# Kernel optimization log

Measured on AMD Instinct MI355X. Metric: run time of the kernel, lower is better.

## Reference

```python
import jax, jax.numpy as jnp
import numpy as np

B, S, D, H = 2, 2048, 1024, 16
HD = D // H  # head_dim = 64


def setup_inputs() -> dict:
    key = jax.random.key(0)
    ks = jax.random.split(key, 9)
    s = 1.0 / np.sqrt(D)
    return {
        "x": jax.random.normal(ks[0], (B, S, D), dtype=jnp.float32),
        "Wq": jax.random.uniform(ks[1], (D, D), jnp.float32, -s, s),
        "bq": jnp.zeros((D,), jnp.float32),
        "Wk": jax.random.uniform(ks[2], (D, D), jnp.float32, -s, s),
        "bk": jnp.zeros((D,), jnp.float32),
        "Wv": jax.random.uniform(ks[3], (D, D), jnp.float32, -s, s),
        "bv": jnp.zeros((D,), jnp.float32),
        "Wo": jax.random.uniform(ks[4], (D, D), jnp.float32, -s, s),
        "bo": jnp.zeros((D,), jnp.float32),
    }


def reference(x, Wq, bq, Wk, bk, Wv, bv, Wo, bo):
    # x: [B,S,D] -> Q/K/V: [B,H,S,HD]
    def heads(t):
        return t.reshape(B, S, H, HD).transpose(0, 2, 1, 3)

    Q = heads(x @ Wq + bq)
    K = heads(x @ Wk + bk)
    V = heads(x @ Wv + bv)
    scale = jnp.sqrt(jnp.asarray(HD, dtype=x.dtype))
    energy = jnp.einsum("bhqd,bhkd->bhqk", Q, K) / scale  # [B,H,S,S]
    attn = jax.nn.softmax(energy, axis=-1)
    # dropout is identity in eval mode
    o = jnp.einsum("bhqk,bhkd->bhqd", attn, V)  # [B,H,S,HD]
    o = o.transpose(0, 2, 1, 3).reshape(B, S, D)
    return o @ Wo + bo
```

## Files before the change

### kernel.cpp

```cpp
#include <hip/hip_runtime.h>
#include <hip/hip_bf16.h>

#define B_  2
#define S_  2048
#define D_  1024
#define H_  16
#define HD_ 64

typedef __attribute__((ext_vector_type(8))) short bf16x8;
typedef __attribute__((ext_vector_type(4))) short bf16x4;
typedef __attribute__((ext_vector_type(4))) float f32x4;

typedef __attribute__((address_space(1))) const short gbl_short;
typedef __attribute__((address_space(3))) short lds_short;

__device__ __forceinline__ short f2bf(float f) {
  union { float f; unsigned u; } v; v.f = f;
  unsigned r = (v.u + 0x7FFFu + ((v.u >> 16) & 1u)) >> 16;
  return (short)r;
}

__device__ __forceinline__ short bf16s(float f) {
  __hip_bfloat16 h = __float2bfloat16(f);
  return *reinterpret_cast<short*>(&h);
}

__global__ __launch_bounds__(256) void cast_x_kernel(const float* __restrict__ x,
                                                     short* __restrict__ xb) {
  int i = blockIdx.x * 256 + threadIdx.x;
  float4 v = ((const float4*)x)[i];
  short4 o;
  o.x = f2bf(v.x); o.y = f2bf(v.y); o.z = f2bf(v.z); o.w = f2bf(v.w);
  ((short4*)xb)[i] = o;
}

__global__ __launch_bounds__(256) void transpose_cast_w(
    const float* __restrict__ w0, const float* __restrict__ w1,
    const float* __restrict__ w2, const float* __restrict__ w3,
    short* __restrict__ t0, short* __restrict__ t1,
    short* __restrict__ t2, short* __restrict__ t3) {
  const float* W = blockIdx.z == 0 ? w0 : blockIdx.z == 1 ? w1 : blockIdx.z == 2 ? w2 : w3;
  short* T       = blockIdx.z == 0 ? t0 : blockIdx.z == 1 ? t1 : blockIdx.z == 2 ? t2 : t3;
  __shared__ float tile[32][33];
  int tx = threadIdx.x, ty = threadIdx.y;
  int x0 = blockIdx.x * 32, y0 = blockIdx.y * 32;
#pragma unroll
  for (int i = 0; i < 4; ++i)
    tile[ty + i * 8][tx] = W[(y0 + ty + i * 8) * D_ + x0 + tx];
  __syncthreads();
#pragma unroll
  for (int i = 0; i < 4; ++i)
    T[(x0 + ty + i * 8) * D_ + y0 + tx] = f2bf(tile[tx][ty + i * 8]);
}

__global__ __launch_bounds__(256) void qkv_gemm(
    const short* __restrict__ xb,
    const short* __restrict__ Wqt, const short* __restrict__ Wkt, const short* __restrict__ Wvt,
    const float* __restrict__ bq, const float* __restrict__ bk, const float* __restrict__ bv,
    short* __restrict__ Qb, short* __restrict__ Kb, short* __restrict__ Vtb) {
  const int which = blockIdx.z;
  const short* Bt   = which == 0 ? Wqt : which == 1 ? Wkt : Wvt;
  const float* bias = which == 0 ? bq  : which == 1 ? bk  : bv;
  const float scl   = which == 0 ? 0.125f * 1.44269504089f : 1.0f;
  const int lane = threadIdx.x & 63, wave = threadIdx.x >> 6;
  const int l15 = lane & 15, quad = lane >> 4;
  const int wm = wave & 1, wn = wave >> 1;
  const int m0 = blockIdx.x * 128, n0 = blockIdx.y * 128;
  const int srow = lane >> 2;
  const int skp  = (((lane & 3) ^ ((srow >> 1) & 3)) * 8);
  const int rsw  = (l15 >> 1) & 3;

  __shared__ short lA[3][128 * 32];
  __shared__ short lB[3][128 * 32];

  f32x4 acc[4][4];
#pragma unroll
  for (int mi = 0; mi < 4; ++mi)
#pragma unroll
    for (int ni = 0; ni < 4; ++ni) { f32x4 z = {0.f, 0.f, 0.f, 0.f}; acc[mi][ni] = z; }

  auto stage = [&](int it, int buf) {
    int kk = it * 32;
#pragma unroll
    for (int j = 0; j < 2; ++j) {
      int c = wave * 2 + j;
      int row = c * 16 + srow;
      __builtin_amdgcn_global_load_lds(
          (gbl_short*)(xb + (m0 + row) * D_ + kk + skp),
          (lds_short*)(&lA[buf][0] + c * 512 + lane * 8), 16, 0, 0);
      __builtin_amdgcn_global_load_lds(
          (gbl_short*)(Bt + (n0 + row) * D_ + kk + skp),
          (lds_short*)(&lB[buf][0] + c * 512 + lane * 8), 16, 0, 0);
    }
  };

  auto compute = [&](int cur) {
    bf16x8 af[4], bf[4];
#pragma unroll
    for (int i = 0; i < 4; ++i) {
      af[i] = *(const bf16x8*)(&lA[cur][0] + (wm * 64 + i * 16 + l15) * 32 + ((quad ^ rsw)) * 8);
      bf[i] = *(const bf16x8*)(&lB[cur][0] + (wn * 64 + i * 16 + l15) * 32 + ((quad ^ rsw)) * 8);
    }
#pragma unroll
    for (int mi = 0; mi < 4; ++mi)
#pragma unroll
      for (int ni = 0; ni < 4; ++ni)
        acc[mi][ni] = __builtin_amdgcn_mfma_f32_16x16x32_bf16(af[mi], bf[ni], acc[mi][ni], 0, 0, 0);
  };

  stage(0, 0);
  stage(1, 1);
  for (int it = 0; it < 30; ++it) {
    stage(it + 2, (it + 2) % 3);
    asm volatile("s_waitcnt vmcnt(8)" ::: "memory");
    __builtin_amdgcn_s_barrier();
    compute(it % 3);
    asm volatile("" ::: "memory");
    __builtin_amdgcn_s_barrier();
  }
  asm volatile("s_waitcnt vmcnt(4)" ::: "memory");
  __builtin_amdgcn_s_barrier();
  compute(0);
  asm volatile("s_waitcnt vmcnt(0)" ::: "memory");
  __builtin_amdgcn_s_barrier();
  compute(1);

#pragma unroll
  for (int mi = 0; mi < 4; ++mi) {
    int m = m0 + wm * 64 + mi * 16 + quad * 4;
    int bb = m >> 11;
    int s0 = m & (S_ - 1);
#pragma unroll
    for (int ni = 0; ni < 4; ++ni) {
      int n = n0 + wn * 64 + ni * 16 + l15;
      int h = n >> 6, hd = n & 63;
      float bsv = bias[n];
      if (which < 2) {
        short* dst = which == 0 ? Qb : Kb;
#pragma unroll
        for (int r = 0; r < 4; ++r)
          dst[((bb * H_ + h) * S_ + (s0 + r)) * HD_ + hd] = f2bf((acc[mi][ni][r] + bsv) * scl);
      } else {
        short4 pk;
        pk.x = f2bf(acc[mi][ni][0] + bsv);
        pk.y = f2bf(acc[mi][ni][1] + bsv);
        pk.z = f2bf(acc[mi][ni][2] + bsv);
        pk.w = f2bf(acc[mi][ni][3] + bsv);
        *(short4*)(Vtb + ((bb * H_ + h) * HD_ + hd) * S_ + s0) = pk;
      }
    }
  }
}

__global__ __launch_bounds__(256) void out_gemm(
    const short* __restrict__ Ob, const short* __restrict__ Wot,
    const float* __restrict__ bo, float* __restrict__ out) {
  const int lane = threadIdx.x & 63, wave = threadIdx.x >> 6;
  const int l15 = lane & 15, quad = lane >> 4;
  const int wm = wave & 1, wn = wave >> 1;
  const int m0 = blockIdx.x * 128, n0 = blockIdx.y * 128;
  const int srow = lane >> 2;
  const int skp  = (((lane & 3) ^ ((srow >> 1) & 3)) * 8);
  const int rsw  = (l15 >> 1) & 3;

  __shared__ short lA[3][128 * 32];
  __shared__ short lB[3][128 * 32];

  f32x4 acc[4][4];
#pragma unroll
  for (int mi = 0; mi < 4; ++mi)
#pragma unroll
    for (int ni = 0; ni < 4; ++ni) { f32x4 z = {0.f, 0.f, 0.f, 0.f}; acc[mi][ni] = z; }

  auto stage = [&](int it, int buf) {
    int kk = it * 32;
#pragma unroll
    for (int j = 0; j < 2; ++j) {
      int c = wave * 2 + j;
      int row = c * 16 + srow;
      __builtin_amdgcn_global_load_lds(
          (gbl_short*)(Ob + (m0 + row) * D_ + kk + skp),
          (lds_short*)(&lA[buf][0] + c * 512 + lane * 8), 16, 0, 0);
      __builtin_amdgcn_global_load_lds(
          (gbl_short*)(Wot + (n0 + row) * D_ + kk + skp),
          (lds_short*)(&lB[buf][0] + c * 512 + lane * 8), 16, 0, 0);
    }
  };

  auto compute = [&](int cur) {
    bf16x8 af[4], bf[4];
#pragma unroll
    for (int i = 0; i < 4; ++i) {
      af[i] = *(const bf16x8*)(&lA[cur][0] + (wm * 64 + i * 16 + l15) * 32 + ((quad ^ rsw)) * 8);
      bf[i] = *(const bf16x8*)(&lB[cur][0] + (wn * 64 + i * 16 + l15) * 32 + ((quad ^ rsw)) * 8);
    }
#pragma unroll
    for (int mi = 0; mi < 4; ++mi)
#pragma unroll
      for (int ni = 0; ni < 4; ++ni)
        acc[mi][ni] = __builtin_amdgcn_mfma_f32_16x16x32_bf16(af[mi], bf[ni], acc[mi][ni], 0, 0, 0);
  };

  stage(0, 0);
  stage(1, 1);
  for (int it = 0; it < 30; ++it) {
    stage(it + 2, (it + 2) % 3);
    asm volatile("s_waitcnt vmcnt(8)" ::: "memory");
    __builtin_amdgcn_s_barrier();
    compute(it % 3);
    asm volatile("" ::: "memory");
    __builtin_amdgcn_s_barrier();
  }
  asm volatile("s_waitcnt vmcnt(4)" ::: "memory");
  __builtin_amdgcn_s_barrier();
  compute(0);
  asm volatile("s_waitcnt vmcnt(0)" ::: "memory");
  __builtin_amdgcn_s_barrier();
  compute(1);

#pragma unroll
  for (int mi = 0; mi < 4; ++mi) {
    int m = m0 + wm * 64 + mi * 16 + quad * 4;
#pragma unroll
    for (int ni = 0; ni < 4; ++ni) {
      int n = n0 + wn * 64 + ni * 16 + l15;
      float bsv = bo[n];
#pragma unroll
      for (int r = 0; r < 4; ++r)
        out[(m + r) * D_ + n] = acc[mi][ni][r] + bsv;
    }
  }
}

__global__ __launch_bounds__(256, 2) void attn_kernel(
    const short* __restrict__ Qb, const short* __restrict__ Kb,
    const short* __restrict__ Vtb, short* __restrict__ Ob) {
  const int qt = blockIdx.x, h = blockIdx.y, b = blockIdx.z;
  const int base = (b * H_ + h) * S_ * HD_;
  const int tid = threadIdx.x;
  const int lane = tid & 63, wave = tid >> 6;
  const int grp = wave >> 1;
  const int wq  = wave & 1;
  const int l15 = lane & 15, quad = lane >> 4;

  __shared__ __align__(16) char smem[33280];
  short* lK = (short*)smem;
  short* lV = (short*)(smem + 16384);

  const int q0 = qt * 128 + wq * 64;

  bf16x8 qf[4][2];
#pragma unroll
  for (int mi = 0; mi < 4; ++mi)
#pragma unroll
    for (int ks = 0; ks < 2; ++ks)
      qf[mi][ks] = *(const bf16x8*)(Qb + base + (q0 + mi * 16 + l15) * HD_ + ks * 32 + quad * 8);

  f32x4 oacc[4][4];
  f32x4 lacc[4];
#pragma unroll
  for (int mi = 0; mi < 4; ++mi) {
    f32x4 z = {0.f, 0.f, 0.f, 0.f};
    lacc[mi] = z;
#pragma unroll
    for (int nb = 0; nb < 4; ++nb) oacc[mi][nb] = z;
  }

  bf16x8 onesf;
#pragma unroll
  for (int i = 0; i < 8; ++i) onesf[i] = (short)0x3F80;

  const int tig = tid & 127;
  const int slotK = tig & 7,  rowK = tig >> 3;
  const int slotV = tig & 3,  rowV = tig >> 2;
  const short* kp = Kb + base + (grp * 1024 + rowK) * HD_ + ((slotK ^ (rowK & 7)) * 8);
  const short* vp = Vtb + base + rowV * S_ + grp * 1024 + ((slotV ^ ((rowV >> 2) & 3)) * 8);
  lds_short* ldk = (lds_short*)(lK + grp * 2048 + tig * 8);
  lds_short* ldv = (lds_short*)(lV + grp * 2048 + tig * 8);

  auto stage = [&](int kt, int buf) {
#pragma unroll
    for (int j = 0; j < 2; ++j) {
      __builtin_amdgcn_global_load_lds((gbl_short*)(kp + kt * 32 * HD_ + j * 16 * HD_),
                                       ldk + buf * 4096 + j * 1024, 16, 0, 0);
      __builtin_amdgcn_global_load_lds((gbl_short*)(vp + kt * 32 + j * 32 * S_),
                                       ldv + buf * 4096 + j * 1024, 16, 0, 0);
    }
  };

  const int swzK = l15 & 7;
  const int fsw  = (l15 >> 2) & 3;
  const int g1 = (quad >> 1) ^ fsw;
  const int g2 = (2 | (quad >> 1)) ^ fsw;
  const int vsub = (quad & 1) * 4;

  stage(0, 0);
  __syncthreads();

  for (int kt = 0; kt < 32; ++kt) {
    const int buf = kt & 1;
    if (kt < 31) stage(kt + 1, buf ^ 1);

    const short* lKc = lK + buf * 4096 + grp * 2048;
    const short* lVc = lV + buf * 4096 + grp * 2048;

    f32x4 sacc[4][2];
#pragma unroll
    for (int mi = 0; mi < 4; ++mi)
#pragma unroll
      for (int nb = 0; nb < 2; ++nb) { f32x4 z = {0.f, 0.f, 0.f, 0.f}; sacc[mi][nb] = z; }
#pragma unroll
    for (int nb = 0; nb < 2; ++nb)
#pragma unroll
      for (int ks = 0; ks < 2; ++ks) {
        bf16x8 kf = *(const bf16x8*)(lKc + (nb * 16 + l15) * 64 + (((ks * 4 + quad) ^ swzK) * 8));
#pragma unroll
        for (int mi = 0; mi < 4; ++mi)
          sacc[mi][nb] = __builtin_amdgcn_mfma_f32_16x16x32_bf16(kf, qf[mi][ks], sacc[mi][nb], 0, 0, 0);
      }

    bf16x8 af[4];
#pragma unroll
    for (int mi = 0; mi < 4; ++mi)
#pragma unroll
      for (int j = 0; j < 8; ++j)
        af[mi][j] = bf16s(__builtin_amdgcn_exp2f(sacc[mi][j >> 2][j & 3]));

#pragma unroll
    for (int nbh = 0; nbh < 4; ++nbh) {
      const short* vrow = lVc + (nbh * 16 + l15) * 32 + vsub;
      bf16x4 v1 = *(const bf16x4*)(vrow + g1 * 8);
      bf16x4 v2 = *(const bf16x4*)(vrow + g2 * 8);
      bf16x8 vf = __builtin_shufflevector(v1, v2, 0, 1, 2, 3, 4, 5, 6, 7);
#pragma unroll
      for (int mi = 0; mi < 4; ++mi)
        oacc[mi][nbh] = __builtin_amdgcn_mfma_f32_16x16x32_bf16(af[mi], vf, oacc[mi][nbh], 0, 0, 0);
    }
#pragma unroll
    for (int mi = 0; mi < 4; ++mi)
      lacc[mi] = __builtin_amdgcn_mfma_f32_16x16x32_bf16(af[mi], onesf, lacc[mi], 0, 0, 0);
    __syncthreads();
  }

  float* exch = (float*)smem;
  float* lex  = (float*)(smem + 32768);
  if (grp == 1) {
#pragma unroll
    for (int mi = 0; mi < 4; ++mi)
#pragma unroll
      for (int nbh = 0; nbh < 4; ++nbh)
#pragma unroll
        for (int r = 0; r < 4; ++r)
          exch[wq * 4096 + (mi * 16 + quad * 4 + r) * 64 + nbh * 16 + l15] = oacc[mi][nbh][r];
    if (l15 == 0) {
#pragma unroll
      for (int mi = 0; mi < 4; ++mi)
#pragma unroll
        for (int r = 0; r < 4; ++r)
          lex[wq * 64 + mi * 16 + quad * 4 + r] = lacc[mi][r];
    }
  }
  __syncthreads();
  if (grp == 0) {
#pragma unroll
    for (int mi = 0; mi < 4; ++mi)
#pragma unroll
      for (int r = 0; r < 4; ++r) {
        int row = mi * 16 + quad * 4 + r;
        float l2 = lex[wq * 64 + row];
        float inv = 1.0f / (lacc[mi][r] + l2);
        int sg = q0 + row;
#pragma unroll
        for (int nbh = 0; nbh < 4; ++nbh) {
          float o2 = exch[wq * 4096 + row * 64 + nbh * 16 + l15];
          Ob[(b * S_ + sg) * D_ + h * HD_ + nbh * 16 + l15] =
              bf16s((oacc[mi][nbh][r] + o2) * inv);
        }
      }
  }
}

extern "C" void kernel_launch(void* const* d_in, const int* in_sizes, int n_in,
                              void* d_out, int out_size, void* d_ws, size_t ws_size,
                              hipStream_t stream) {
  (void)in_sizes; (void)n_in; (void)out_size; (void)ws_size;
  const float* x  = (const float*)d_in[0];
  const float* Wq = (const float*)d_in[1];
  const float* bq = (const float*)d_in[2];
  const float* Wk = (const float*)d_in[3];
  const float* bk = (const float*)d_in[4];
  const float* Wv = (const float*)d_in[5];
  const float* bv = (const float*)d_in[6];
  const float* Wo = (const float*)d_in[7];
  const float* bo = (const float*)d_in[8];
  float* out = (float*)d_out;

  char* ws = (char*)d_ws;
  short* xb  = (short*)(ws);
  short* Wqt = (short*)(ws + 8388608);
  short* Wkt = Wqt + 1048576;
  short* Wvt = Wkt + 1048576;
  short* Wot = Wvt + 1048576;
  short* Qb  = Wot + 1048576;
  short* Kb  = Qb + 4194304;
  short* Vtb = Kb + 4194304;
  short* Ob  = Vtb + 4194304;

  cast_x_kernel<<<4096, 256, 0, stream>>>(x, xb);
  transpose_cast_w<<<dim3(32, 32, 4), dim3(32, 8), 0, stream>>>(
      Wq, Wk, Wv, Wo, Wqt, Wkt, Wvt, Wot);
  qkv_gemm<<<dim3(32, 8, 3), 256, 0, stream>>>(
      xb, Wqt, Wkt, Wvt, bq, bk, bv, Qb, Kb, Vtb);
  attn_kernel<<<dim3(16, 16, 2), 256, 0, stream>>>(Qb, Kb, Vtb, Ob);
  out_gemm<<<dim3(32, 8), 256, 0, stream>>>(Ob, Wot, bo, out);
}
```

Measured before the change: 188.2 us.

## Triple-buffer attention K/V staging with vmcnt waits, XCD-aware block mapping, setprio

The attention kernel's K/V staging moves from a double buffer with a full __syncthreads per tile to a three-deep ring buffer. Explicit s_waitcnt vmcnt counts and raw barriers let loads run two tiles ahead of compute. The grid is flattened to 1D and remapped so the blocks of each (batch, head) pair land on the same XCD, aiming for better L2 reuse of K/V. s_setprio is raised around the MFMA sections. LDS grows to 48KB, which may limit occupancy. The hand-counted vmcnt values are fragile if the compiler reorders loads.

```diff
diff --git a/kernel.cpp b/kernel.cpp
--- a/kernel.cpp
+++ b/kernel.cpp
@@ -235,7 +235,12 @@
 __global__ __launch_bounds__(256, 2) void attn_kernel(
     const short* __restrict__ Qb, const short* __restrict__ Kb,
     const short* __restrict__ Vtb, short* __restrict__ Ob) {
-  const int qt = blockIdx.x, h = blockIdx.y, b = blockIdx.z;
+  const int id = blockIdx.x;
+  const int xcd = id & 7;
+  const int slot = id >> 3;
+  const int pr = xcd * 4 + (slot >> 4);
+  const int qt = slot & 15;
+  const int h = pr & 15, b = pr >> 4;
   const int base = (b * H_ + h) * S_ * HD_;
   const int tid = threadIdx.x;
   const int lane = tid & 63, wave = tid >> 6;
@@ -243,9 +248,9 @@
   const int wq  = wave & 1;
   const int l15 = lane & 15, quad = lane >> 4;
 
-  __shared__ __align__(16) char smem[33280];
+  __shared__ __align__(16) char smem[49152];
   short* lK = (short*)smem;
-  short* lV = (short*)(smem + 16384);
+  short* lV = (short*)(smem + 24576);
 
   const int q0 = qt * 128 + wq * 64;
 
@@ -294,13 +299,7 @@
   const int g2 = (2 | (quad >> 1)) ^ fsw;
   const int vsub = (quad & 1) * 4;
 
-  stage(0, 0);
-  __syncthreads();
-
-  for (int kt = 0; kt < 32; ++kt) {
-    const int buf = kt & 1;
-    if (kt < 31) stage(kt + 1, buf ^ 1);
-
+  auto compute = [&](int buf) {
     const short* lKc = lK + buf * 4096 + grp * 2048;
     const short* lVc = lV + buf * 4096 + grp * 2048;
 
@@ -309,6 +308,7 @@
     for (int mi = 0; mi < 4; ++mi)
 #pragma unroll
       for (int nb = 0; nb < 2; ++nb) { f32x4 z = {0.f, 0.f, 0.f, 0.f}; sacc[mi][nb] = z; }
+    __builtin_amdgcn_s_setprio(1);
 #pragma unroll
     for (int nb = 0; nb < 2; ++nb)
 #pragma unroll
@@ -318,6 +318,7 @@
         for (int mi = 0; mi < 4; ++mi)
           sacc[mi][nb] = __builtin_amdgcn_mfma_f32_16x16x32_bf16(kf, qf[mi][ks], sacc[mi][nb], 0, 0, 0);
       }
+    __builtin_amdgcn_s_setprio(0);
 
     bf16x8 af[4];
 #pragma unroll
@@ -326,6 +327,7 @@
       for (int j = 0; j < 8; ++j)
         af[mi][j] = bf16s(__builtin_amdgcn_exp2f(sacc[mi][j >> 2][j & 3]));
 
+    __builtin_amdgcn_s_setprio(1);
 #pragma unroll
     for (int nbh = 0; nbh < 4; ++nbh) {
       const short* vrow = lVc + (nbh * 16 + l15) * 32 + vsub;
@@ -339,8 +341,29 @@
 #pragma unroll
     for (int mi = 0; mi < 4; ++mi)
       lacc[mi] = __builtin_amdgcn_mfma_f32_16x16x32_bf16(af[mi], onesf, lacc[mi], 0, 0, 0);
-    __syncthreads();
-  }
+    __builtin_amdgcn_s_setprio(0);
+  };
+
+  asm volatile("s_waitcnt vmcnt(0)" ::: "memory");
+  stage(0, 0);
+  stage(1, 1);
+
+  for (int kt = 0; kt < 30; ++kt) {
+    stage(kt + 2, (kt + 2) % 3);
+    asm volatile("s_waitcnt vmcnt(8)" ::: "memory");
+    __builtin_amdgcn_s_barrier();
+    compute(kt % 3);
+    asm volatile("" ::: "memory");
+    __builtin_amdgcn_s_barrier();
+  }
+  asm volatile("s_waitcnt vmcnt(4)" ::: "memory");
+  __builtin_amdgcn_s_barrier();
+  compute(0);
+  asm volatile("s_waitcnt vmcnt(0)" ::: "memory");
+  __builtin_amdgcn_s_barrier();
+  compute(1);
+
+  __syncthreads();
 
   float* exch = (float*)smem;
   float* lex  = (float*)(smem + 32768);
@@ -411,6 +434,6 @@
       Wq, Wk, Wv, Wo, Wqt, Wkt, Wvt, Wot);
   qkv_gemm<<<dim3(32, 8, 3), 256, 0, stream>>>(
       xb, Wqt, Wkt, Wvt, bq, bk, bv, Qb, Kb, Vtb);
-  attn_kernel<<<dim3(16, 16, 2), 256, 0, stream>>>(Qb, Kb, Vtb, Ob);
+  attn_kernel<<<512, 256, 0, stream>>>(Qb, Kb, Vtb, Ob);
   out_gemm<<<dim3(32, 8), 256, 0, stream>>>(Ob, Wot, bo, out);
 }
```

After: 187.4 us. About the same (-0.4%).
